# Optimization experiments

Measured on AMD Instinct MI355X. Metric: run time of the kernel, lower is better.

Reference implementation:

```python
import jax, jax.numpy as jnp
import numpy as np
import math

E, K, CAPF = 8, 2, 1.25
D, DFF = 512, 2048


def setup_inputs() -> dict:
    key = jax.random.key(0)
    ks = jax.random.split(key, 5)
    s = lambda k, sh, sc: (jax.random.normal(k, sh, jnp.float32) * sc)
    return {
        "x": jax.random.normal(ks[0], (8, 4096, D), jnp.float32),
        "Wr": s(ks[1], (D, E), 1.0 / math.sqrt(D)),
        "br": jnp.zeros((E,), jnp.float32),
        "W1": s(ks[2], (E, D, DFF), 1.0 / math.sqrt(D)),
        "b1": jnp.zeros((E, DFF), jnp.float32),
        "W2": s(ks[3], (E, DFF, D), 1.0 / math.sqrt(DFF)),
        "b2": jnp.zeros((E, D), jnp.float32),
    }


def _moe(x, Wr, br, W1, b1, W2, b2):
    orig = x.shape
    d = orig[-1]
    xf = x.reshape(-1, d)                     # [N, d]
    N = xf.shape[0]
    # --- TopK router ---
    logits = xf @ Wr + br                      # [N, E]
    probs = jax.nn.softmax(logits, axis=-1)
    topk_p, topk_i = jax.lax.top_k(probs, K)   # [N, K]
    topk_w = topk_p / (jnp.sum(topk_p, axis=-1, keepdims=True) + 1e-9)
    # --- Capacity-based sparse dispatch ---
    cap = max(1, int(math.ceil(CAPF * float(N * K) / float(E))))
    flat_e = topk_i.reshape(-1)                # [N*K] expert id per slot
    flat_w = topk_w.reshape(-1)                # [N*K]
    tok = jnp.repeat(jnp.arange(N), K)         # [N*K] source token id
    one_hot = jax.nn.one_hot(flat_e, E, dtype=xf.dtype)          # [N*K, E]
    pos = (jnp.cumsum(one_hot, axis=0) - one_hot)[jnp.arange(N * K), flat_e]
    pos = pos.astype(jnp.int32)                # position within expert buffer
    keep = pos < cap                           # tokens beyond capacity dropped
    w_k = jnp.where(keep, flat_w, 0.0)
    sum_w = jnp.zeros((N,), xf.dtype).at[tok].add(w_k)           # kept weight per token
    w_norm = w_k / (sum_w[tok] + 1e-9)
    slot = flat_e * cap + pos                  # flat index into [E*cap]
    slot_safe = jnp.where(keep, slot, E * cap) # out-of-bounds -> dropped by scatter
    expert_in = (jnp.zeros((E * cap, d), xf.dtype)
                 .at[slot_safe].set(xf[tok], mode="drop")
                 .reshape(E, cap, d))
    # --- Grouped expert FFN (exact GELU like torch nn.GELU) ---
    h = jax.nn.gelu(jnp.einsum("ecd,edf->ecf", expert_in, W1) + b1[:, None, :],
                    approximate=False)
    expert_out = (jnp.einsum("ecf,efd->ecd", h, W2) + b2[:, None, :]).reshape(E * cap, d)
    # --- Combine: gather back and weighted scatter-add per token ---
    contrib = expert_out[jnp.where(keep, slot, 0)]               # dropped -> w_norm=0
    y = jnp.zeros((N, d), xf.dtype).at[tok].add(contrib * w_norm[:, None])
    return y.reshape(orig)


def reference(x, Wr, br, W1, b1, W2, b2):
    return _moe(x, Wr, br, W1, b1, W2, b2)
```

## Files before the change

kernel.cpp:

```cpp
#include <hip/hip_runtime.h>
#include <cstdint>
#include <cstddef>

#define E_EXP 8
#define TOPK 2
#define DMODEL 512
#define DFFDIM 2048

typedef __attribute__((ext_vector_type(8))) short short8;
typedef __attribute__((ext_vector_type(4))) float f32x4;

__device__ __forceinline__ unsigned short f2bf(float f) {
    unsigned int u = __float_as_uint(f);
    u += 0x7fffu + ((u >> 16) & 1u);
    return (unsigned short)(u >> 16);
}

__device__ __forceinline__ void gld_lds16(const unsigned short* g, unsigned short* l) {
    __builtin_amdgcn_global_load_lds(
        (const __attribute__((address_space(1))) void*)g,
        (__attribute__((address_space(3))) void*)l, 16, 0, 0);
}

__global__ __launch_bounds__(256) void transpose_kernel(
    const float* __restrict__ in, unsigned short* __restrict__ out, int R, int C)
{
    __shared__ float tile[32][33];
    const float* ie = in + (size_t)blockIdx.z * R * C;
    unsigned short* oe = out + (size_t)blockIdx.z * R * C;
    int x = blockIdx.x * 32 + threadIdx.x;
#pragma unroll
    for (int i = 0; i < 4; i++) {
        int ry = blockIdx.y * 32 + threadIdx.y + i * 8;
        tile[threadIdx.y + i * 8][threadIdx.x] = ie[(size_t)ry * C + x];
    }
    __syncthreads();
    int xo = blockIdx.y * 32 + threadIdx.x;
#pragma unroll
    for (int i = 0; i < 4; i++) {
        int co = blockIdx.x * 32 + threadIdx.y + i * 8;
        oe[(size_t)co * R + xo] = f2bf(tile[threadIdx.x][threadIdx.y + i * 8]);
    }
}

__global__ __launch_bounds__(256) void router_kernel(
    const float* __restrict__ x, const float* __restrict__ Wr,
    const float* __restrict__ br, int N,
    int* __restrict__ e0e1, float2* __restrict__ w01)
{
    int lane = threadIdx.x & 63, wave = threadIdx.x >> 6;
    int t = blockIdx.x * 4 + wave;
    if (t >= N) return;
    const float* xr = x + (size_t)t * DMODEL;
    float4 v0 = *(const float4*)(xr + lane * 4);
    float4 v1 = *(const float4*)(xr + 256 + lane * 4);
    float xv[8] = {v0.x, v0.y, v0.z, v0.w, v1.x, v1.y, v1.z, v1.w};
    const float* wr0 = Wr + (size_t)lane * 32;
    const float* wr1 = Wr + (size_t)(256 + lane * 4) * 8;
    double acc[8];
#pragma unroll
    for (int j = 0; j < 8; j++) acc[j] = 0.0;
#pragma unroll
    for (int c = 0; c < 4; c++) {
#pragma unroll
        for (int j = 0; j < 8; j++) {
            acc[j] += (double)xv[c] * (double)wr0[c * 8 + j];
            acc[j] += (double)xv[4 + c] * (double)wr1[c * 8 + j];
        }
    }
#pragma unroll
    for (int j = 0; j < 8; j++) {
        double s = acc[j];
#pragma unroll
        for (int o = 32; o > 0; o >>= 1) s += __shfl_xor(s, o, 64);
        acc[j] = s;
    }
    if (lane == 0) {
        float l[8], p[8];
        float mx = -1e30f;
        for (int j = 0; j < 8; j++) { l[j] = (float)acc[j] + br[j]; mx = fmaxf(mx, l[j]); }
        float Z = 0.f;
        for (int j = 0; j < 8; j++) { p[j] = expf(l[j] - mx); Z += p[j]; }
        for (int j = 0; j < 8; j++) p[j] /= Z;
        int e0 = 0;
        for (int j = 1; j < 8; j++) if (l[j] > l[e0]) e0 = j;
        int e1 = (e0 == 0) ? 1 : 0;
        for (int j = 0; j < 8; j++) if (j != e0 && l[j] > l[e1]) e1 = j;
        float den = p[e0] + p[e1] + 1e-9f;
        e0e1[t] = e0 | (e1 << 8);
        w01[t] = make_float2(p[e0] / den, p[e1] / den);
    }
}

__global__ __launch_bounds__(256) void hist_kernel(
    const int* __restrict__ e0e1, int NK, int* __restrict__ hist)
{
    __shared__ int cnt[8];
    int t = threadIdx.x;
    if (t < 8) cnt[t] = 0;
    __syncthreads();
    int s = blockIdx.x * 256 + t;
    if (s < NK) {
        int pk = e0e1[s >> 1];
        int e = (s & 1) ? ((pk >> 8) & 255) : (pk & 255);
        atomicAdd(&cnt[e], 1);
    }
    __syncthreads();
    if (t < 8) hist[blockIdx.x * 8 + t] = cnt[t];
}

__global__ __launch_bounds__(256) void scan_kernel(
    const int* __restrict__ hist, int NB, int cap,
    int* __restrict__ base, int* __restrict__ cnt_used)
{
    __shared__ int buf[256];
    int t = threadIdx.x;
    for (int e = 0; e < 8; e++) {
        int v = (t < NB) ? hist[t * 8 + e] : 0;
        int val = v;
        buf[t] = val;
        __syncthreads();
        for (int o = 1; o < 256; o <<= 1) {
            int add = (t >= o) ? buf[t - o] : 0;
            __syncthreads();
            val += add;
            buf[t] = val;
            __syncthreads();
        }
        if (t < NB) base[t * 8 + e] = val - v;
        if (t == 255) cnt_used[e] = min(val, cap);
        __syncthreads();
    }
}

__global__ __launch_bounds__(256) void pos_kernel(
    const int* __restrict__ e0e1, const float2* __restrict__ w01,
    const int* __restrict__ base, int NK, int cap,
    int* __restrict__ tok_of, float* __restrict__ wslot)
{
    __shared__ int waveCnt[4][8];
    __shared__ float kw[256];
    int t = threadIdx.x, lane = t & 63, wave = t >> 6;
    int s = blockIdx.x * 256 + t;
    bool valid = s < NK;
    int e = 8; float w = 0.f;
    if (valid) {
        int pk = e0e1[s >> 1];
        float2 ww = w01[s >> 1];
        if (s & 1) { e = (pk >> 8) & 255; w = ww.y; }
        else       { e = pk & 255;        w = ww.x; }
    }
    unsigned long long mymask = 0ull;
#pragma unroll
    for (int j = 0; j < 8; j++) {
        unsigned long long m = __ballot(e == j);
        if (lane == j) waveCnt[wave][j] = __popcll(m);
        if (e == j) mymask = m;
    }
    __syncthreads();
    int wrank = __popcll(mymask & ((1ull << lane) - 1ull));
    int prior = 0;
    for (int w2 = 0; w2 < wave; w2++) prior += waveCnt[w2][e & 7];
    int pos = base[blockIdx.x * 8 + (e & 7)] + prior + wrank;
    bool keep = valid && (pos < cap);
    kw[t] = keep ? w : 0.f;
    __syncthreads();
    float sum = kw[t] + kw[t ^ 1];
    float wn = keep ? (kw[t] / (sum + 1e-9f)) : 0.f;
    if (keep) {
        int si = e * cap + pos;
        tok_of[si] = s >> 1;
        wslot[si] = wn;
    }
}

__global__ __launch_bounds__(512, 2) void fused_ffn_kernel(
    const float* __restrict__ x,
    const unsigned short* __restrict__ W1t,
    const float* __restrict__ b1,
    const unsigned short* __restrict__ W2t,
    const float* __restrict__ b2,
    float* __restrict__ y,
    const int* __restrict__ cnt, const int* __restrict__ tok_of,
    const float* __restrict__ wslot, int cap)
{
    __shared__ unsigned short Wb[2][32768];
    __shared__ unsigned short Hlds[8 * 640];

    int b = blockIdx.x;
    int e = b & 7, mtile = b >> 3;
    int m0 = mtile * 128;
    int M = cnt[e];
    if (m0 >= M) return;

    int t = threadIdx.x, lane = t & 63, w = t >> 6;
    int lr = lane & 15, lq = lane >> 4;

    const unsigned short* W1e = W1t + (size_t)e * DFFDIM * DMODEL;
    const unsigned short* W2e = W2t + (size_t)e * DMODEL * DFFDIM;

    int mrowA = m0 + w * 16 + lr;
    int tokA = (mrowA < M) ? tok_of[e * cap + mrowA] : -1;
    const float* xr = x + (size_t)(tokA < 0 ? 0 : tokA) * DMODEL;
    short8 a_frag[16];
#pragma unroll
    for (int kf = 0; kf < 16; kf++) {
        float4 u0 = *(const float4*)(xr + kf * 32 + lq * 8);
        float4 u1 = *(const float4*)(xr + kf * 32 + lq * 8 + 4);
        short8 f;
        f[0] = (short)f2bf(u0.x); f[1] = (short)f2bf(u0.y);
        f[2] = (short)f2bf(u0.z); f[3] = (short)f2bf(u0.w);
        f[4] = (short)f2bf(u1.x); f[5] = (short)f2bf(u1.y);
        f[6] = (short)f2bf(u1.z); f[7] = (short)f2bf(u1.w);
        if (tokA < 0) f = (short8){0, 0, 0, 0, 0, 0, 0, 0};
        a_frag[kf] = f;
    }

    f32x4 yac[32];
#pragma unroll
    for (int j = 0; j < 32; j++) yac[j] = (f32x4){0.f, 0.f, 0.f, 0.f};

    unsigned short* Hl = Hlds + w * 640;
    int l2 = lane >> 2;
    int w2seg = (((lane & 3) ^ (l2 & 3)) * 8);
    int w1seg = (lane ^ w) * 8;

    {
        int f0 = 0;
#pragma unroll
        for (int q = 0; q < 4; q++) {
            int f = q * 8 + w;
            gld_lds16(W1e + (size_t)(f0 + f) * DMODEL + w1seg,
                      &Wb[0][q * 4096 + w * 512]);
            int n = q * 128 + w * 16 + l2;
            gld_lds16(W2e + (size_t)n * DFFDIM + f0 + w2seg,
                      &Wb[0][16384 + q * 4096 + w * 512]);
        }
    }
    __syncthreads();

    int buf = 0;
    for (int c = 0; c < 64; c++) {
        if (c < 63) {
            int f0 = (c + 1) * 32;
#pragma unroll
            for (int q = 0; q < 4; q++) {
                int f = q * 8 + w;
                gld_lds16(W1e + (size_t)(f0 + f) * DMODEL + w1seg,
                          &Wb[buf ^ 1][q * 4096 + w * 512]);
                int n = q * 128 + w * 16 + l2;
                gld_lds16(W2e + (size_t)n * DFFDIM + f0 + w2seg,
                          &Wb[buf ^ 1][16384 + q * 4096 + w * 512]);
            }
        }
        const unsigned short* W1b = &Wb[buf][0];
        const unsigned short* W2b = &Wb[buf][16384];
        f32x4 h0 = (f32x4){0.f, 0.f, 0.f, 0.f};
        f32x4 h1 = (f32x4){0.f, 0.f, 0.f, 0.f};
#pragma unroll
        for (int kf = 0; kf < 16; kf++) {
            int s6 = ((kf * 4 + lq) ^ (lr & 7)) * 8;
            short8 bf0 = *(const short8*)(W1b + lr * 512 + s6);
            short8 bf1 = *(const short8*)(W1b + (16 + lr) * 512 + s6);
            h0 = __builtin_amdgcn_mfma_f32_16x16x32_bf16(a_frag[kf], bf0, h0, 0, 0, 0);
            h1 = __builtin_amdgcn_mfma_f32_16x16x32_bf16(a_frag[kf], bf1, h1, 0, 0, 0);
        }
        int f0 = c * 32;
        float b1v0 = b1[e * DFFDIM + f0 + lr];
        float b1v1 = b1[e * DFFDIM + f0 + 16 + lr];
#pragma unroll
        for (int r = 0; r < 4; r++) {
            float v0 = h0[r] + b1v0;
            v0 = 0.5f * v0 * (1.0f + erff(v0 * 0.7071067811865475f));
            float v1 = h1[r] + b1v1;
            v1 = 0.5f * v1 * (1.0f + erff(v1 * 0.7071067811865475f));
            Hl[(lq * 4 + r) * 40 + lr] = f2bf(v0);
            Hl[(lq * 4 + r) * 40 + 16 + lr] = f2bf(v1);
        }
        short8 a2 = *(const short8*)(Hl + lr * 40 + lq * 8);
#pragma unroll
        for (int j = 0; j < 32; j++) {
            short8 b2f = *(const short8*)(W2b + (16 * j + lr) * 32 + ((lq ^ (lr & 3)) * 8));
            yac[j] = __builtin_amdgcn_mfma_f32_16x16x32_bf16(a2, b2f, yac[j], 0, 0, 0);
        }
        __syncthreads();
        buf ^= 1;
    }

    int tokC[4]; float wC[4];
#pragma unroll
    for (int r = 0; r < 4; r++) {
        int m = m0 + w * 16 + lq * 4 + r;
        if (m < M) { tokC[r] = tok_of[e * cap + m]; wC[r] = wslot[e * cap + m]; }
        else       { tokC[r] = -1; wC[r] = 0.f; }
    }
#pragma unroll
    for (int j = 0; j < 32; j++) {
        int n = 16 * j + lr;
        float b2v = b2[e * DMODEL + n];
        f32x4 v = yac[j];
#pragma unroll
        for (int r = 0; r < 4; r++) {
            if (tokC[r] >= 0)
                atomicAdd(y + (size_t)tokC[r] * DMODEL + n, wC[r] * (v[r] + b2v));
        }
    }
}

extern "C" void kernel_launch(void* const* d_in, const int* in_sizes, int n_in,
                              void* d_out, int out_size, void* d_ws, size_t ws_size,
                              hipStream_t stream)
{
    const float* x  = (const float*)d_in[0];
    const float* Wr = (const float*)d_in[1];
    const float* br = (const float*)d_in[2];
    const float* W1 = (const float*)d_in[3];
    const float* b1 = (const float*)d_in[4];
    const float* W2 = (const float*)d_in[5];
    const float* b2 = (const float*)d_in[6];
    float* y = (float*)d_out;
    (void)n_in; (void)ws_size;

    const int N = in_sizes[0] / DMODEL;
    const int NK = N * TOPK;
    const int cap = (NK * 5 + 31) / 32;
    const int NB = (NK + 255) / 256;
    const int mT = cap / 128;

    char* ws = (char*)d_ws;
    size_t off = 0;
    auto take = [&](size_t bytes) {
        char* p = ws + off;
        off = (off + bytes + 255) & ~(size_t)255;
        return p;
    };
    unsigned short* W1t = (unsigned short*)take((size_t)E_EXP * DMODEL * DFFDIM * 2);
    unsigned short* W2t = (unsigned short*)take((size_t)E_EXP * DMODEL * DFFDIM * 2);
    int*    e0e1 = (int*)take((size_t)N * 4);
    float2* w01  = (float2*)take((size_t)N * 8);
    int*    hist = (int*)take((size_t)NB * 8 * 4);
    int*    base = (int*)take((size_t)NB * 8 * 4);
    int*    cnt  = (int*)take(64);
    int*    tok_of = (int*)take((size_t)E_EXP * cap * 4);
    float*  wslot  = (float*)take((size_t)E_EXP * cap * 4);

    transpose_kernel<<<dim3(DFFDIM / 32, DMODEL / 32, E_EXP), dim3(32, 8), 0, stream>>>(W1, W1t, DMODEL, DFFDIM);
    transpose_kernel<<<dim3(DMODEL / 32, DFFDIM / 32, E_EXP), dim3(32, 8), 0, stream>>>(W2, W2t, DFFDIM, DMODEL);
    router_kernel<<<(N + 3) / 4, 256, 0, stream>>>(x, Wr, br, N, e0e1, w01);
    hist_kernel<<<NB, 256, 0, stream>>>(e0e1, NK, hist);
    scan_kernel<<<1, 256, 0, stream>>>(hist, NB, cap, base, cnt);
    pos_kernel<<<NB, 256, 0, stream>>>(e0e1, w01, base, NK, cap, tok_of, wslot);
    hipMemsetAsync(d_out, 0, (size_t)out_size * 4, stream);

    fused_ffn_kernel<<<E_EXP * mT, 512, 0, stream>>>(
        x, W1t, b1, W2t, b2, y, cnt, tok_of, wslot, cap);
}
```

Measured before the change: 1.075 ms.

## Split weight staging into single W1/W2 buffers with phase-offset prefetch

```diff
diff --git a/kernel.cpp b/kernel.cpp
--- a/kernel.cpp
+++ b/kernel.cpp
@@ -184,8 +184,9 @@
     const int* __restrict__ cnt, const int* __restrict__ tok_of,
     const float* __restrict__ wslot, int cap)
 {
-    __shared__ unsigned short Wb[2][32768];
-    __shared__ unsigned short Hlds[8 * 640];
+    __shared__ unsigned short W1s[16384];
+    __shared__ unsigned short W2s[16384];
+    __shared__ unsigned int   Hb[8 * 320];
 
     int b = blockIdx.x;
     int e = b & 7, mtile = b >> 3;
@@ -220,71 +221,67 @@
 #pragma unroll
     for (int j = 0; j < 32; j++) yac[j] = (f32x4){0.f, 0.f, 0.f, 0.f};
 
-    unsigned short* Hl = Hlds + w * 640;
-    int l2 = lane >> 2;
-    int w2seg = (((lane & 3) ^ (l2 & 3)) * 8);
-    int w1seg = (lane ^ w) * 8;
-
-    {
-        int f0 = 0;
-#pragma unroll
-        for (int q = 0; q < 4; q++) {
-            int f = q * 8 + w;
-            gld_lds16(W1e + (size_t)(f0 + f) * DMODEL + w1seg,
-                      &Wb[0][q * 4096 + w * 512]);
-            int n = q * 128 + w * 16 + l2;
-            gld_lds16(W2e + (size_t)n * DFFDIM + f0 + w2seg,
-                      &Wb[0][16384 + q * 4096 + w * 512]);
-        }
-    }
-    __syncthreads();
-
-    int buf = 0;
+    int wofs = __builtin_amdgcn_readfirstlane(w * 512);
+    const unsigned short* gW1 = W1e + (size_t)w * DMODEL + (size_t)(lane ^ w) * 8;
+    const unsigned short* gW2 = W2e + (size_t)(w * 16 + (lane >> 2)) * DFFDIM
+                                    + (size_t)((lane & 3) ^ ((lane >> 2) & 3)) * 8;
+
+#pragma unroll
+    for (int q = 0; q < 4; q++) {
+        gld_lds16(gW1 + (size_t)q * 4096,   W1s + q * 4096 + wofs);
+        gld_lds16(gW2 + (size_t)q * 262144, W2s + q * 4096 + wofs);
+    }
+    __syncthreads();
+
+    const unsigned short* W1r0 = W1s + (2 * lr) * 512;
+    int s1a = (2 * lr) & 7, s1b = s1a | 1;
+    unsigned int* Hw = Hb + w * 320;
+    const unsigned short* Hu = (const unsigned short*)(Hb + w * 320 + lr * 20) + lq * 8;
+    const unsigned short* W2r = W2s + lr * 32 + ((lq ^ (lr & 3)) * 8);
+
     for (int c = 0; c < 64; c++) {
-        if (c < 63) {
-            int f0 = (c + 1) * 32;
-#pragma unroll
-            for (int q = 0; q < 4; q++) {
-                int f = q * 8 + w;
-                gld_lds16(W1e + (size_t)(f0 + f) * DMODEL + w1seg,
-                          &Wb[buf ^ 1][q * 4096 + w * 512]);
-                int n = q * 128 + w * 16 + l2;
-                gld_lds16(W2e + (size_t)n * DFFDIM + f0 + w2seg,
-                          &Wb[buf ^ 1][16384 + q * 4096 + w * 512]);
-            }
-        }
-        const unsigned short* W1b = &Wb[buf][0];
-        const unsigned short* W2b = &Wb[buf][16384];
         f32x4 h0 = (f32x4){0.f, 0.f, 0.f, 0.f};
         f32x4 h1 = (f32x4){0.f, 0.f, 0.f, 0.f};
 #pragma unroll
         for (int kf = 0; kf < 16; kf++) {
-            int s6 = ((kf * 4 + lq) ^ (lr & 7)) * 8;
-            short8 bf0 = *(const short8*)(W1b + lr * 512 + s6);
-            short8 bf1 = *(const short8*)(W1b + (16 + lr) * 512 + s6);
+            int k4 = kf * 4 + lq;
+            short8 bf0 = *(const short8*)(W1r0 + ((k4 ^ s1a) * 8));
+            short8 bf1 = *(const short8*)(W1r0 + 512 + ((k4 ^ s1b) * 8));
             h0 = __builtin_amdgcn_mfma_f32_16x16x32_bf16(a_frag[kf], bf0, h0, 0, 0, 0);
             h1 = __builtin_amdgcn_mfma_f32_16x16x32_bf16(a_frag[kf], bf1, h1, 0, 0, 0);
         }
-        int f0 = c * 32;
-        float b1v0 = b1[e * DFFDIM + f0 + lr];
-        float b1v1 = b1[e * DFFDIM + f0 + 16 + lr];
-#pragma unroll
-        for (int r = 0; r < 4; r++) {
-            float v0 = h0[r] + b1v0;
-            v0 = 0.5f * v0 * (1.0f + erff(v0 * 0.7071067811865475f));
-            float v1 = h1[r] + b1v1;
-            v1 = 0.5f * v1 * (1.0f + erff(v1 * 0.7071067811865475f));
-            Hl[(lq * 4 + r) * 40 + lr] = f2bf(v0);
-            Hl[(lq * 4 + r) * 40 + 16 + lr] = f2bf(v1);
-        }
-        short8 a2 = *(const short8*)(Hl + lr * 40 + lq * 8);
+        __syncthreads();
+        if (c < 63) {
+            const unsigned short* g1 = gW1 + (size_t)(c + 1) * 16384;
+#pragma unroll
+            for (int q = 0; q < 4; q++)
+                gld_lds16(g1 + (size_t)q * 4096, W1s + q * 4096 + wofs);
+        }
+        {
+            float2 b1v = *(const float2*)(b1 + e * DFFDIM + c * 32 + 2 * lr);
+#pragma unroll
+            for (int r = 0; r < 4; r++) {
+                float v0 = h0[r] + b1v.x;
+                v0 = 0.5f * v0 * (1.0f + erff(v0 * 0.7071067811865475f));
+                float v1 = h1[r] + b1v.y;
+                v1 = 0.5f * v1 * (1.0f + erff(v1 * 0.7071067811865475f));
+                Hw[(lq * 4 + r) * 20 + lr] =
+                    (unsigned int)f2bf(v0) | ((unsigned int)f2bf(v1) << 16);
+            }
+        }
+        short8 a2 = *(const short8*)Hu;
 #pragma unroll
         for (int j = 0; j < 32; j++) {
-            short8 b2f = *(const short8*)(W2b + (16 * j + lr) * 32 + ((lq ^ (lr & 3)) * 8));
+            short8 b2f = *(const short8*)(W2r + j * 512);
             yac[j] = __builtin_amdgcn_mfma_f32_16x16x32_bf16(a2, b2f, yac[j], 0, 0, 0);
         }
         __syncthreads();
-        buf ^= 1;
+        if (c < 63) {
+            const unsigned short* g2 = gW2 + (size_t)(c + 1) * 32;
+#pragma unroll
+            for (int q = 0; q < 4; q++)
+                gld_lds16(g2 + (size_t)q * 262144, W2s + q * 4096 + wofs);
+        }
     }
 
     int tokC[4]; float wC[4];
```

Result: no change. 1.061 ms (-1.2%).
